# Kernel tuning notes

Measured on AMD Instinct MI355X. Metric: run time of the kernel, lower is better.

The kernel has to match this reference:

```python
import jax, jax.numpy as jnp
import numpy as np


def setup_inputs() -> dict:
    key = jax.random.key(0)
    k1, k2, k3, k4 = jax.random.split(key, 4)
    B, T, C, H = 32, 2048, 384, 64
    x = jax.random.normal(k1, (B, T, C), dtype=jnp.float32)
    # nn.Linear(C, H, bias=False): weight stored [H, C], applied as x @ W.T.
    # We store the transposed [C, H] form directly.
    s = 1.0 / np.sqrt(C)
    Wk = jax.random.normal(k2, (C, H), dtype=jnp.float32) * s
    Wq = jax.random.normal(k3, (C, H), dtype=jnp.float32) * s
    Wv = jax.random.normal(k4, (C, H), dtype=jnp.float32) * s
    return {"x": x, "Wk": Wk, "Wq": Wq, "Wv": Wv}


def reference(x, Wk, Wq, Wv):
    # x: [B, T, C]; Wk/Wq/Wv: [C, H]
    T = x.shape[1]
    H = Wk.shape[1]
    k = jnp.einsum('btc,ch->bth', x, Wk)
    q = jnp.einsum('btc,ch->bth', x, Wq)
    v = jnp.einsum('btc,ch->bth', x, Wv)
    scale = H ** (-0.5)
    scores = jnp.einsum('bth,bsh->bts', q, k) * scale  # [B, T, T]
    causal = jnp.tril(jnp.ones((T, T), dtype=bool))
    scores = jnp.where(causal, scores, -jnp.inf)
    attn = jax.nn.softmax(scores, axis=-1)
    # dropout is identity in eval mode
    out = jnp.einsum('bts,bsh->bth', attn, v)  # [B, T, H]
    return out
```

## Files before the change

kernel.cpp:

```cpp
#include <hip/hip_runtime.h>

typedef __bf16 bf16_8 __attribute__((ext_vector_type(8)));
typedef __bf16 bf16_4 __attribute__((ext_vector_type(4)));
typedef float  f32x4  __attribute__((ext_vector_type(4)));

#define NB 32
#define NT 2048
#define NC 384
#define NH 64

static __device__ __forceinline__ f32x4 mfma16(bf16_8 a, bf16_8 b, f32x4 c) {
  return __builtin_amdgcn_mfma_f32_16x16x32_bf16(a, b, c, 0, 0, 0);
}

__global__ void pack_w_kernel(const float* __restrict__ Wk, const float* __restrict__ Wq,
                              const float* __restrict__ Wv, __bf16* __restrict__ Wt) {
  int idx = blockIdx.x * 256 + threadIdx.x;
  if (idx >= 192 * NC) return;
  int n = idx / NC, k = idx % NC;
  int sel = n >> 6, h = n & 63;
  const float* W = (sel == 0) ? Wq : (sel == 1 ? Wk : Wv);
  float v = W[k * NH + h];
  if (sel == 0) v *= 0.125f * 1.44269504088896340736f;
  Wt[idx] = (__bf16)v;
}

__launch_bounds__(1024, 4)
__global__ void qkv_kernel(const float* __restrict__ x, const __bf16* __restrict__ Wt,
                           __bf16* __restrict__ Q, __bf16* __restrict__ K,
                           __bf16* __restrict__ Vt) {
  __shared__ __bf16 Wl[192 * 384];

  const int tid  = threadIdx.x;
  const int lane = tid & 63, wq = tid >> 6;
  const int quad = lane >> 4, l16 = lane & 15;
  const int rowblk = blockIdx.x * 256;
  const int rbase  = rowblk + wq * 16;
  const int row    = rbase + l16;

  #pragma unroll
  for (int i = 0; i < 9; ++i) {
    int g = tid + i * 1024;
    int r = g / 48, c = g - r * 48;
    int p = c ^ (r & 7);
    uint4 v = ((const uint4*)Wt)[g];
    *(uint4*)&Wl[(r * 48 + p) * 8] = v;
  }
  __syncthreads();

  f32x4 acc[12];
  #pragma unroll
  for (int n = 0; n < 12; ++n) acc[n] = f32x4{0.f, 0.f, 0.f, 0.f};

  const float* xrow = x + (size_t)row * NC;
  f32x4 x0 = *(const f32x4*)(xrow + quad * 8);
  f32x4 x1 = *(const f32x4*)(xrow + quad * 8 + 4);

  #pragma unroll
  for (int kc = 0; kc < 12; ++kc) {
    f32x4 nx0, nx1;
    if (kc < 11) {
      const float* xp = xrow + (kc + 1) * 32 + quad * 8;
      nx0 = *(const f32x4*)xp;
      nx1 = *(const f32x4*)(xp + 4);
    }
    bf16_8 a;
    a[0] = (__bf16)x0[0]; a[1] = (__bf16)x0[1]; a[2] = (__bf16)x0[2]; a[3] = (__bf16)x0[3];
    a[4] = (__bf16)x1[0]; a[5] = (__bf16)x1[1]; a[6] = (__bf16)x1[2]; a[7] = (__bf16)x1[3];
    const int pc = (kc * 4 + quad) ^ (l16 & 7);
    const int cbase = l16 * 48 + pc;
    #pragma unroll
    for (int n = 0; n < 12; ++n) {
      bf16_8 b = *(const bf16_8*)&Wl[(n * 16 * 48 + cbase) * 8];
      acc[n] = mfma16(a, b, acc[n]);
    }
    x0 = nx0; x1 = nx1;
  }

  __syncthreads();
  __bf16 (*Qs)[72]  = (__bf16(*)[72])Wl;
  __bf16 (*Ks2)[72] = (__bf16(*)[72])(Wl + 18432);
  __bf16 (*Vl)[264] = (__bf16(*)[264])(Wl + 36864);

  #pragma unroll
  for (int n = 0; n < 4; ++n)
    #pragma unroll
    for (int r = 0; r < 4; ++r) {
      int t = wq * 16 + quad * 4 + r;
      int h = n * 16 + l16;
      Qs[t][h]  = (__bf16)acc[n][r];
      Ks2[t][h] = (__bf16)acc[n + 4][r];
    }
  #pragma unroll
  for (int n = 8; n < 12; ++n) {
    int h = (n - 8) * 16 + l16;
    int t0 = wq * 16 + quad * 4;
    bf16_4 p;
    p[0] = (__bf16)acc[n][0]; p[1] = (__bf16)acc[n][1];
    p[2] = (__bf16)acc[n][2]; p[3] = (__bf16)acc[n][3];
    *(bf16_4*)&Vl[h][t0] = p;
  }
  __syncthreads();

  {
    int t = tid >> 2, h0 = (tid & 3) * 16;
    __bf16* qdst = Q + (size_t)(rowblk + t) * NH + h0;
    __bf16* kdst = K + (size_t)(rowblk + t) * NH + h0;
    const __bf16* qsrc = &Qs[t][h0];
    const __bf16* ksrc = &Ks2[t][h0];
    ((uint4*)qdst)[0] = ((const uint4*)qsrc)[0];
    ((uint4*)qdst)[1] = ((const uint4*)qsrc)[1];
    ((uint4*)kdst)[0] = ((const uint4*)ksrc)[0];
    ((uint4*)kdst)[1] = ((const uint4*)ksrc)[1];
  }
  {
    int h = tid >> 4, seg = tid & 15;
    int bb = rowblk >> 11, t0 = (rowblk & (NT - 1)) + seg * 16;
    const __bf16* src = &Vl[h][seg * 16];
    __bf16* dst = Vt + ((size_t)(bb * NH + h)) * NT + t0;
    ((uint4*)dst)[0] = ((const uint4*)src)[0];
    ((uint4*)dst)[1] = ((const uint4*)src)[1];
  }
}

__launch_bounds__(256)
__global__ void attn_kernel(const __bf16* __restrict__ Q, const __bf16* __restrict__ K,
                            const __bf16* __restrict__ Vt, float* __restrict__ out) {
  __shared__ __bf16 Ks[2][64][72];
  __shared__ __bf16 Vs[2][64][72];

  const int tid  = threadIdx.x;
  const int lane = tid & 63, wq = tid >> 6;
  const int quad = lane >> 4, l16 = lane & 15;
  const int b    = blockIdx.x >> 4;
  const int pair = blockIdx.x & 15;

  const float NEG_INF = -__builtin_inff();
  const float RTHR = 8.f;
  const int r = tid >> 2, seg = tid & 3;
  const __bf16* Kg = K  + (size_t)b * NT * NH;
  const __bf16* Vg = Vt + (size_t)b * NH * NT;

  const int c0 = seg * 4;
  const int kp0 = ((c0 & 8) << 2) + ((c0 & 3) << 3) + (((c0 >> 2) & 1) << 2);
  const int kp1 = (((c0+1) & 8) << 2) + (((c0+1) & 3) << 3) + ((((c0+1) >> 2) & 1) << 2);
  const int kp2 = (((c0+2) & 8) << 2) + (((c0+2) & 3) << 3) + ((((c0+2) >> 2) & 1) << 2);
  const int kp3 = (((c0+3) & 8) << 2) + (((c0+3) & 3) << 3) + ((((c0+3) >> 2) & 1) << 2);

  for (int pass = 0; pass < 2; ++pass) {
    const int qt = pass ? pair : (31 - pair);
    const int q0 = qt * 64;
    const int nIter = qt + 1;

    const __bf16* qrow = Q + ((size_t)(b * NT + q0 + wq * 16 + l16)) * NH + quad * 8;
    bf16_8 qf0 = *(const bf16_8*)qrow;
    bf16_8 qf1 = *(const bf16_8*)(qrow + 32);

    f32x4 o[4];
    #pragma unroll
    for (int i = 0; i < 4; ++i) o[i] = f32x4{0.f, 0.f, 0.f, 0.f};
    float m_i = NEG_INF;
    float l_i = 0.f;

    __syncthreads();

    {
      const uint4* sK = (const uint4*)(Kg + (size_t)r * NH + seg * 16);
      uint4 ka = sK[0], kb = sK[1];
      const uint4* sV = (const uint4*)(Vg + (size_t)r * NT + seg * 16);
      uint4 va = sV[0], vb = sV[1];
      *(uint4*)&Ks[0][r][seg * 16]     = ka;
      *(uint4*)&Ks[0][r][seg * 16 + 8] = kb;
      *(uint2*)&Vs[0][r][kp0] = make_uint2(va.x, va.y);
      *(uint2*)&Vs[0][r][kp1] = make_uint2(va.z, va.w);
      *(uint2*)&Vs[0][r][kp2] = make_uint2(vb.x, vb.y);
      *(uint2*)&Vs[0][r][kp3] = make_uint2(vb.z, vb.w);
    }

    for (int i = 0; i < nIter; ++i) {
      const int cur = i & 1;
      const bool more = (i + 1 < nIter);
      uint4 nka, nkb, nva, nvb;
      if (more) {
        const int s0n = (i + 1) * 64;
        const uint4* sK = (const uint4*)(Kg + (size_t)(s0n + r) * NH + seg * 16);
        nka = sK[0]; nkb = sK[1];
        const uint4* sV = (const uint4*)(Vg + (size_t)r * NT + s0n + seg * 16);
        nva = sV[0]; nvb = sV[1];
      }
      __syncthreads();

      f32x4 s[4];
      __builtin_amdgcn_s_setprio(1);
      #pragma unroll
      for (int st = 0; st < 4; ++st) {
        bf16_8 a0 = *(const bf16_8*)&Ks[cur][st * 16 + l16][quad * 8];
        bf16_8 a1 = *(const bf16_8*)&Ks[cur][st * 16 + l16][quad * 8 + 32];
        f32x4 accv = f32x4{0.f, 0.f, 0.f, 0.f};
        accv = mfma16(a0, qf0, accv);
        accv = mfma16(a1, qf1, accv);
        s[st] = accv;
      }
      __builtin_amdgcn_s_setprio(0);

      if (i == qt) {
        int qg = wq * 16 + l16;
        #pragma unroll
        for (int st = 0; st < 4; ++st)
          #pragma unroll
          for (int rr = 0; rr < 4; ++rr) {
            int sg = st * 16 + quad * 4 + rr;
            if (sg > qg) s[st][rr] = NEG_INF;
          }
      }

      float t0 = fmaxf(fmaxf(s[0][0], s[0][1]), fmaxf(s[0][2], s[0][3]));
      float t1 = fmaxf(fmaxf(s[1][0], s[1][1]), fmaxf(s[1][2], s[1][3]));
      float t2 = fmaxf(fmaxf(s[2][0], s[2][1]), fmaxf(s[2][2], s[2][3]));
      float t3 = fmaxf(fmaxf(s[3][0], s[3][1]), fmaxf(s[3][2], s[3][3]));
      float mxl = fmaxf(fmaxf(t0, t1), fmaxf(t2, t3));

      if (__any(mxl - m_i > RTHR)) {
        float mrow = fmaxf(mxl, __shfl_xor(mxl, 16));
        mrow = fmaxf(mrow, __shfl_xor(mrow, 32));
        float m_new = fmaxf(m_i, mrow);
        float alpha = exp2f(m_i - m_new);
        f32x4 av;
        #pragma unroll
        for (int rr = 0; rr < 4; ++rr) av[rr] = __shfl(alpha, quad * 4 + rr);
        #pragma unroll
        for (int nt = 0; nt < 4; ++nt)
          #pragma unroll
          for (int rr = 0; rr < 4; ++rr) o[nt][rr] *= av[rr];
        l_i *= alpha;
        m_i = m_new;
      }

      float ls[4];
      bf16_8 pa0, pa1;
      #pragma unroll
      for (int st = 0; st < 4; ++st) {
        float lp = 0.f;
        #pragma unroll
        for (int rr = 0; rr < 4; ++rr) {
          float p = exp2f(s[st][rr] - m_i);
          lp += p;
          __bf16 pb = (__bf16)p;
          if (st < 2) pa0[st * 4 + rr] = pb;
          else        pa1[(st - 2) * 4 + rr] = pb;
        }
        ls[st] = lp;
      }
      l_i += (ls[0] + ls[1]) + (ls[2] + ls[3]);

      __builtin_amdgcn_s_setprio(1);
      #pragma unroll
      for (int nt = 0; nt < 4; ++nt) {
        bf16_8 b0 = *(const bf16_8*)&Vs[cur][nt * 16 + l16][quad * 8];
        bf16_8 b1 = *(const bf16_8*)&Vs[cur][nt * 16 + l16][quad * 8 + 32];
        o[nt] = mfma16(pa0, b0, o[nt]);
        o[nt] = mfma16(pa1, b1, o[nt]);
      }
      __builtin_amdgcn_s_setprio(0);

      if (more) {
        *(uint4*)&Ks[1 - cur][r][seg * 16]     = nka;
        *(uint4*)&Ks[1 - cur][r][seg * 16 + 8] = nkb;
        *(uint2*)&Vs[1 - cur][r][kp0] = make_uint2(nva.x, nva.y);
        *(uint2*)&Vs[1 - cur][r][kp1] = make_uint2(nva.z, nva.w);
        *(uint2*)&Vs[1 - cur][r][kp2] = make_uint2(nvb.x, nvb.y);
        *(uint2*)&Vs[1 - cur][r][kp3] = make_uint2(nvb.z, nvb.w);
      }
    }

    float lt = l_i;
    lt += __shfl_xor(lt, 16);
    lt += __shfl_xor(lt, 32);
    f32x4 lv;
    #pragma unroll
    for (int rr = 0; rr < 4; ++rr) lv[rr] = 1.f / __shfl(lt, quad * 4 + rr);
    float* op = out + ((size_t)(b * NT + q0 + wq * 16 + quad * 4)) * NH + l16;
    #pragma unroll
    for (int nt = 0; nt < 4; ++nt)
      #pragma unroll
      for (int rr = 0; rr < 4; ++rr)
        op[(size_t)rr * NH + nt * 16] = o[nt][rr] * lv[rr];
  }
}

extern "C" void kernel_launch(void* const* d_in, const int* in_sizes, int n_in,
                              void* d_out, int out_size, void* d_ws, size_t ws_size,
                              hipStream_t stream) {
  const float* x  = (const float*)d_in[0];
  const float* Wk = (const float*)d_in[1];
  const float* Wq = (const float*)d_in[2];
  const float* Wv = (const float*)d_in[3];
  float* out = (float*)d_out;

  char* ws = (char*)d_ws;
  __bf16* Wt  = (__bf16*)ws;
  __bf16* Qb  = (__bf16*)(ws + 256 * 1024);
  __bf16* Kb  = Qb + (size_t)NB * NT * NH;
  __bf16* Vtb = Kb + (size_t)NB * NT * NH;

  pack_w_kernel<<<288, 256, 0, stream>>>(Wk, Wq, Wv, Wt);
  qkv_kernel<<<256, 1024, 0, stream>>>(x, Wt, Qb, Kb, Vtb);
  attn_kernel<<<NB * 16, 256, 0, stream>>>(Qb, Kb, Vtb, out);
}
```

Measured before the change: 208.7 us.

## Process 128-row query tiles per block with two 16-row chunks per wave

Each wave now handles 32 query rows as two 16-row MFMA chunks, so a block covers 128 query rows and every K/V tile staged in shared memory feeds twice as many MFMAs. This halves K/V global and LDS traffic per query and halves the grid to 256 blocks, still pairing light and heavy causal tiles. The cost is higher register pressure, fewer blocks than the 256 CUs can comfortably balance, and more masking work on the last two diagonal tiles.

```diff
diff --git a/kernel.cpp b/kernel.cpp
--- a/kernel.cpp
+++ b/kernel.cpp
@@ -132,8 +132,8 @@
   const int tid  = threadIdx.x;
   const int lane = tid & 63, wq = tid >> 6;
   const int quad = lane >> 4, l16 = lane & 15;
-  const int b    = blockIdx.x >> 4;
-  const int pair = blockIdx.x & 15;
+  const int b    = blockIdx.x >> 3;
+  const int pairId = blockIdx.x & 7;
 
   const float NEG_INF = -__builtin_inff();
   const float RTHR = 8.f;
@@ -148,19 +148,26 @@
   const int kp3 = (((c0+3) & 8) << 2) + (((c0+3) & 3) << 3) + ((((c0+3) >> 2) & 1) << 2);
 
   for (int pass = 0; pass < 2; ++pass) {
-    const int qt = pass ? pair : (31 - pair);
-    const int q0 = qt * 64;
-    const int nIter = qt + 1;
-
-    const __bf16* qrow = Q + ((size_t)(b * NT + q0 + wq * 16 + l16)) * NH + quad * 8;
-    bf16_8 qf0 = *(const bf16_8*)qrow;
-    bf16_8 qf1 = *(const bf16_8*)(qrow + 32);
-
-    f32x4 o[4];
-    #pragma unroll
-    for (int i = 0; i < 4; ++i) o[i] = f32x4{0.f, 0.f, 0.f, 0.f};
-    float m_i = NEG_INF;
-    float l_i = 0.f;
+    const int j = pass ? pairId : (15 - pairId);
+    const int q0 = j * 128;
+    const int nIter = 2 * j + 2;
+    const int qloc = wq * 32 + l16;
+
+    bf16_8 qf0[2], qf1[2];
+    #pragma unroll
+    for (int qc = 0; qc < 2; ++qc) {
+      const __bf16* qrow = Q + ((size_t)(b * NT + q0 + wq * 32 + qc * 16 + l16)) * NH + quad * 8;
+      qf0[qc] = *(const bf16_8*)qrow;
+      qf1[qc] = *(const bf16_8*)(qrow + 32);
+    }
+
+    f32x4 o[4][2];
+    #pragma unroll
+    for (int nt = 0; nt < 4; ++nt)
+      #pragma unroll
+      for (int qc = 0; qc < 2; ++qc) o[nt][qc] = f32x4{0.f, 0.f, 0.f, 0.f};
+    float m_i[2] = {NEG_INF, NEG_INF};
+    float l_i[2] = {0.f, 0.f};
 
     __syncthreads();
 
@@ -190,76 +197,89 @@
       }
       __syncthreads();
 
-      f32x4 s[4];
+      f32x4 s[4][2];
       __builtin_amdgcn_s_setprio(1);
       #pragma unroll
       for (int st = 0; st < 4; ++st) {
         bf16_8 a0 = *(const bf16_8*)&Ks[cur][st * 16 + l16][quad * 8];
         bf16_8 a1 = *(const bf16_8*)&Ks[cur][st * 16 + l16][quad * 8 + 32];
-        f32x4 accv = f32x4{0.f, 0.f, 0.f, 0.f};
-        accv = mfma16(a0, qf0, accv);
-        accv = mfma16(a1, qf1, accv);
-        s[st] = accv;
+        #pragma unroll
+        for (int qc = 0; qc < 2; ++qc) {
+          f32x4 accv = f32x4{0.f, 0.f, 0.f, 0.f};
+          accv = mfma16(a0, qf0[qc], accv);
+          accv = mfma16(a1, qf1[qc], accv);
+          s[st][qc] = accv;
+        }
       }
       __builtin_amdgcn_s_setprio(0);
 
-      if (i == qt) {
-        int qg = wq * 16 + l16;
-        #pragma unroll
-        for (int st = 0; st < 4; ++st)
+      if (i >= nIter - 2) {
+        const int sBase = i * 64 - j * 128;
+        #pragma unroll
+        for (int qc = 0; qc < 2; ++qc) {
+          const int ql = qloc + qc * 16;
+          #pragma unroll
+          for (int st = 0; st < 4; ++st)
+            #pragma unroll
+            for (int rr = 0; rr < 4; ++rr) {
+              int sg = sBase + st * 16 + quad * 4 + rr;
+              if (sg > ql) s[st][qc][rr] = NEG_INF;
+            }
+        }
+      }
+
+      bf16_8 pa0[2], pa1[2];
+      #pragma unroll
+      for (int qc = 0; qc < 2; ++qc) {
+        float t0 = fmaxf(fmaxf(s[0][qc][0], s[0][qc][1]), fmaxf(s[0][qc][2], s[0][qc][3]));
+        float t1 = fmaxf(fmaxf(s[1][qc][0], s[1][qc][1]), fmaxf(s[1][qc][2], s[1][qc][3]));
+        float t2 = fmaxf(fmaxf(s[2][qc][0], s[2][qc][1]), fmaxf(s[2][qc][2], s[2][qc][3]));
+        float t3 = fmaxf(fmaxf(s[3][qc][0], s[3][qc][1]), fmaxf(s[3][qc][2], s[3][qc][3]));
+        float mxl = fmaxf(fmaxf(t0, t1), fmaxf(t2, t3));
+
+        if (__any(mxl - m_i[qc] > RTHR)) {
+          float mrow = fmaxf(mxl, __shfl_xor(mxl, 16));
+          mrow = fmaxf(mrow, __shfl_xor(mrow, 32));
+          float m_new = fmaxf(m_i[qc], mrow);
+          float alpha = exp2f(m_i[qc] - m_new);
+          f32x4 av;
+          #pragma unroll
+          for (int rr = 0; rr < 4; ++rr) av[rr] = __shfl(alpha, quad * 4 + rr);
+          #pragma unroll
+          for (int nt = 0; nt < 4; ++nt)
+            #pragma unroll
+            for (int rr = 0; rr < 4; ++rr) o[nt][qc][rr] *= av[rr];
+          l_i[qc] *= alpha;
+          m_i[qc] = m_new;
+        }
+
+        float ls[4];
+        #pragma unroll
+        for (int st = 0; st < 4; ++st) {
+          float lp = 0.f;
           #pragma unroll
           for (int rr = 0; rr < 4; ++rr) {
-            int sg = st * 16 + quad * 4 + rr;
-            if (sg > qg) s[st][rr] = NEG_INF;
+            float p = exp2f(s[st][qc][rr] - m_i[qc]);
+            lp += p;
+            __bf16 pb = (__bf16)p;
+            if (st < 2) pa0[qc][st * 4 + rr] = pb;
+            else        pa1[qc][(st - 2) * 4 + rr] = pb;
           }
-      }
-
-      float t0 = fmaxf(fmaxf(s[0][0], s[0][1]), fmaxf(s[0][2], s[0][3]));
-      float t1 = fmaxf(fmaxf(s[1][0], s[1][1]), fmaxf(s[1][2], s[1][3]));
-      float t2 = fmaxf(fmaxf(s[2][0], s[2][1]), fmaxf(s[2][2], s[2][3]));
-      float t3 = fmaxf(fmaxf(s[3][0], s[3][1]), fmaxf(s[3][2], s[3][3]));
-      float mxl = fmaxf(fmaxf(t0, t1), fmaxf(t2, t3));
-
-      if (__any(mxl - m_i > RTHR)) {
-        float mrow = fmaxf(mxl, __shfl_xor(mxl, 16));
-        mrow = fmaxf(mrow, __shfl_xor(mrow, 32));
-        float m_new = fmaxf(m_i, mrow);
-        float alpha = exp2f(m_i - m_new);
-        f32x4 av;
-        #pragma unroll
-        for (int rr = 0; rr < 4; ++rr) av[rr] = __shfl(alpha, quad * 4 + rr);
-        #pragma unroll
-        for (int nt = 0; nt < 4; ++nt)
-          #pragma unroll
-          for (int rr = 0; rr < 4; ++rr) o[nt][rr] *= av[rr];
-        l_i *= alpha;
-        m_i = m_new;
-      }
-
-      float ls[4];
-      bf16_8 pa0, pa1;
-      #pragma unroll
-      for (int st = 0; st < 4; ++st) {
-        float lp = 0.f;
-        #pragma unroll
-        for (int rr = 0; rr < 4; ++rr) {
-          float p = exp2f(s[st][rr] - m_i);
-          lp += p;
-          __bf16 pb = (__bf16)p;
-          if (st < 2) pa0[st * 4 + rr] = pb;
-          else        pa1[(st - 2) * 4 + rr] = pb;
-        }
-        ls[st] = lp;
-      }
-      l_i += (ls[0] + ls[1]) + (ls[2] + ls[3]);
+          ls[st] = lp;
+        }
+        l_i[qc] += (ls[0] + ls[1]) + (ls[2] + ls[3]);
+      }
 
       __builtin_amdgcn_s_setprio(1);
       #pragma unroll
       for (int nt = 0; nt < 4; ++nt) {
         bf16_8 b0 = *(const bf16_8*)&Vs[cur][nt * 16 + l16][quad * 8];
         bf16_8 b1 = *(const bf16_8*)&Vs[cur][nt * 16 + l16][quad * 8 + 32];
-        o[nt] = mfma16(pa0, b0, o[nt]);
-        o[nt] = mfma16(pa1, b1, o[nt]);
+        #pragma unroll
+        for (int qc = 0; qc < 2; ++qc) {
+          o[nt][qc] = mfma16(pa0[qc], b0, o[nt][qc]);
+          o[nt][qc] = mfma16(pa1[qc], b1, o[nt][qc]);
+        }
       }
       __builtin_amdgcn_s_setprio(0);
 
@@ -273,18 +293,21 @@
       }
     }
 
-    float lt = l_i;
-    lt += __shfl_xor(lt, 16);
-    lt += __shfl_xor(lt, 32);
-    f32x4 lv;
-    #pragma unroll
-    for (int rr = 0; rr < 4; ++rr) lv[rr] = 1.f / __shfl(lt, quad * 4 + rr);
-    float* op = out + ((size_t)(b * NT + q0 + wq * 16 + quad * 4)) * NH + l16;
-    #pragma unroll
-    for (int nt = 0; nt < 4; ++nt)
-      #pragma unroll
-      for (int rr = 0; rr < 4; ++rr)
-        op[(size_t)rr * NH + nt * 16] = o[nt][rr] * lv[rr];
+    #pragma unroll
+    for (int qc = 0; qc < 2; ++qc) {
+      float lt = l_i[qc];
+      lt += __shfl_xor(lt, 16);
+      lt += __shfl_xor(lt, 32);
+      f32x4 lv;
+      #pragma unroll
+      for (int rr = 0; rr < 4; ++rr) lv[rr] = 1.f / __shfl(lt, quad * 4 + rr);
+      float* op = out + ((size_t)(b * NT + q0 + wq * 32 + qc * 16 + quad * 4)) * NH + l16;
+      #pragma unroll
+      for (int nt = 0; nt < 4; ++nt)
+        #pragma unroll
+        for (int rr = 0; rr < 4; ++rr)
+          op[(size_t)rr * NH + nt * 16] = o[nt][qc][rr] * lv[rr];
+    }
   }
 }
 
@@ -305,5 +328,5 @@
 
   pack_w_kernel<<<288, 256, 0, stream>>>(Wk, Wq, Wv, Wt);
   qkv_kernel<<<256, 1024, 0, stream>>>(x, Wt, Qb, Kb, Vtb);
-  attn_kernel<<<NB * 16, 256, 0, stream>>>(Qb, Kb, Vtb, out);
-}
+  attn_kernel<<<NB * 8, 256, 0, stream>>>(Qb, Kb, Vtb, out);
+}
```

New measurement: 219.4 us. 5.1% more time.

## Enlarge attention query tile to 128 rows with 512-thread blocks sharing K/V tiles

Applied to the files above, without the earlier changes.

Each attention block now runs 8 waves over 128 query rows instead of 4 waves over 64. The K/V tiles staged in shared memory are reused by twice as many waves, and each thread loads half as much per tile, which cuts global and LDS fill traffic per query row. The causal mask now covers the last two key tiles. In the final tile, the waves for the first 64 query rows compute fully masked scores, which is wasted work. The grid halves to 256 blocks, so each block carries more work and the number of blocks in flight changes.

```diff
diff --git a/kernel.cpp b/kernel.cpp
--- a/kernel.cpp
+++ b/kernel.cpp
@@ -123,7 +123,7 @@
   }
 }
 
-__launch_bounds__(256)
+__launch_bounds__(512)
 __global__ void attn_kernel(const __bf16* __restrict__ Q, const __bf16* __restrict__ K,
                             const __bf16* __restrict__ Vt, float* __restrict__ out) {
   __shared__ __bf16 Ks[2][64][72];
@@ -132,25 +132,25 @@
   const int tid  = threadIdx.x;
   const int lane = tid & 63, wq = tid >> 6;
   const int quad = lane >> 4, l16 = lane & 15;
-  const int b    = blockIdx.x >> 4;
-  const int pair = blockIdx.x & 15;
+  const int b      = blockIdx.x >> 3;
+  const int pairId = blockIdx.x & 7;
 
   const float NEG_INF = -__builtin_inff();
   const float RTHR = 8.f;
-  const int r = tid >> 2, seg = tid & 3;
+  const int r = tid >> 3, seg = tid & 7;
   const __bf16* Kg = K  + (size_t)b * NT * NH;
   const __bf16* Vg = Vt + (size_t)b * NH * NT;
 
-  const int c0 = seg * 4;
-  const int kp0 = ((c0 & 8) << 2) + ((c0 & 3) << 3) + (((c0 >> 2) & 1) << 2);
-  const int kp1 = (((c0+1) & 8) << 2) + (((c0+1) & 3) << 3) + ((((c0+1) >> 2) & 1) << 2);
-  const int kp2 = (((c0+2) & 8) << 2) + (((c0+2) & 3) << 3) + ((((c0+2) >> 2) & 1) << 2);
-  const int kp3 = (((c0+3) & 8) << 2) + (((c0+3) & 3) << 3) + ((((c0+3) >> 2) & 1) << 2);
+  const int c0 = seg * 2;
+  const int kpA = ((c0 & 8) << 2) + ((c0 & 3) << 3) + (((c0 >> 2) & 1) << 2);
+  const int c1 = c0 + 1;
+  const int kpB = ((c1 & 8) << 2) + ((c1 & 3) << 3) + (((c1 >> 2) & 1) << 2);
 
   for (int pass = 0; pass < 2; ++pass) {
-    const int qt = pass ? pair : (31 - pair);
-    const int q0 = qt * 64;
-    const int nIter = qt + 1;
+    const int j = pass ? pairId : (15 - pairId);
+    const int q0 = j * 128;
+    const int nIter = 2 * j + 2;
+    const int qloc = wq * 16 + l16;
 
     const __bf16* qrow = Q + ((size_t)(b * NT + q0 + wq * 16 + l16)) * NH + quad * 8;
     bf16_8 qf0 = *(const bf16_8*)qrow;
@@ -165,28 +165,21 @@
     __syncthreads();
 
     {
-      const uint4* sK = (const uint4*)(Kg + (size_t)r * NH + seg * 16);
-      uint4 ka = sK[0], kb = sK[1];
-      const uint4* sV = (const uint4*)(Vg + (size_t)r * NT + seg * 16);
-      uint4 va = sV[0], vb = sV[1];
-      *(uint4*)&Ks[0][r][seg * 16]     = ka;
-      *(uint4*)&Ks[0][r][seg * 16 + 8] = kb;
-      *(uint2*)&Vs[0][r][kp0] = make_uint2(va.x, va.y);
-      *(uint2*)&Vs[0][r][kp1] = make_uint2(va.z, va.w);
-      *(uint2*)&Vs[0][r][kp2] = make_uint2(vb.x, vb.y);
-      *(uint2*)&Vs[0][r][kp3] = make_uint2(vb.z, vb.w);
+      uint4 ka = *(const uint4*)(Kg + (size_t)r * NH + seg * 8);
+      uint4 va = *(const uint4*)(Vg + (size_t)r * NT + seg * 8);
+      *(uint4*)&Ks[0][r][seg * 8] = ka;
+      *(uint2*)&Vs[0][r][kpA] = make_uint2(va.x, va.y);
+      *(uint2*)&Vs[0][r][kpB] = make_uint2(va.z, va.w);
     }
 
     for (int i = 0; i < nIter; ++i) {
       const int cur = i & 1;
       const bool more = (i + 1 < nIter);
-      uint4 nka, nkb, nva, nvb;
+      uint4 nka, nva;
       if (more) {
         const int s0n = (i + 1) * 64;
-        const uint4* sK = (const uint4*)(Kg + (size_t)(s0n + r) * NH + seg * 16);
-        nka = sK[0]; nkb = sK[1];
-        const uint4* sV = (const uint4*)(Vg + (size_t)r * NT + s0n + seg * 16);
-        nva = sV[0]; nvb = sV[1];
+        nka = *(const uint4*)(Kg + (size_t)(s0n + r) * NH + seg * 8);
+        nva = *(const uint4*)(Vg + (size_t)r * NT + s0n + seg * 8);
       }
       __syncthreads();
 
@@ -203,14 +196,14 @@
       }
       __builtin_amdgcn_s_setprio(0);
 
-      if (i == qt) {
-        int qg = wq * 16 + l16;
+      if (i >= nIter - 2) {
+        const int sBase = i * 64 - j * 128;
         #pragma unroll
         for (int st = 0; st < 4; ++st)
           #pragma unroll
           for (int rr = 0; rr < 4; ++rr) {
-            int sg = st * 16 + quad * 4 + rr;
-            if (sg > qg) s[st][rr] = NEG_INF;
+            int sg = sBase + st * 16 + quad * 4 + rr;
+            if (sg > qloc) s[st][rr] = NEG_INF;
           }
       }
 
@@ -264,12 +257,9 @@
       __builtin_amdgcn_s_setprio(0);
 
       if (more) {
-        *(uint4*)&Ks[1 - cur][r][seg * 16]     = nka;
-        *(uint4*)&Ks[1 - cur][r][seg * 16 + 8] = nkb;
-        *(uint2*)&Vs[1 - cur][r][kp0] = make_uint2(nva.x, nva.y);
-        *(uint2*)&Vs[1 - cur][r][kp1] = make_uint2(nva.z, nva.w);
-        *(uint2*)&Vs[1 - cur][r][kp2] = make_uint2(nvb.x, nvb.y);
-        *(uint2*)&Vs[1 - cur][r][kp3] = make_uint2(nvb.z, nvb.w);
+        *(uint4*)&Ks[1 - cur][r][seg * 8] = nka;
+        *(uint2*)&Vs[1 - cur][r][kpA] = make_uint2(nva.x, nva.y);
+        *(uint2*)&Vs[1 - cur][r][kpB] = make_uint2(nva.z, nva.w);
       }
     }
 
@@ -305,5 +295,5 @@
 
   pack_w_kernel<<<288, 256, 0, stream>>>(Wk, Wq, Wv, Wt);
   qkv_kernel<<<256, 1024, 0, stream>>>(x, Wt, Qb, Kb, Vtb);
-  attn_kernel<<<NB * 16, 256, 0, stream>>>(Qb, Kb, Vtb, out);
-}
+  attn_kernel<<<NB * 8, 512, 0, stream>>>(Qb, Kb, Vtb, out);
+}
```

Result: no change. 207.9 us (-0.4%).
